# Kernel optimization log

Hardware: AMD Instinct MI355X
Metric: run time of the kernel (lower is better)

The kernel has to match this reference:

```python
import jax, jax.numpy as jnp
import numpy as np

N, C, H, W = 64, 64, 8, 8   # batch, channels (img_net_out_dim), feature-map HxW
E = 256                      # ques_rnn_hidden_dim
G = 512                      # rn_g_dim
FD = 512                     # rn_f_dim
GIN = 2 * (C + 2) + E        # g-MLP input dim = 388
NUM_CLASSES = 2


def _lin(key, din, dout):
    # kaiming-uniform-like init for a Linear stored as (in, out)
    bound = float(np.sqrt(6.0 / din))
    w = jax.random.uniform(key, (din, dout), minval=-bound, maxval=bound, dtype=jnp.float32)
    b = jnp.zeros((dout,), dtype=jnp.float32)
    return w, b


def setup_inputs() -> dict:
    key = jax.random.key(0)
    ks = jax.random.split(key, 9)
    img = jax.random.normal(ks[0], (N, C, H, W), dtype=jnp.float32)
    ques = jax.random.normal(ks[1], (N, E), dtype=jnp.float32)
    g_w1, g_b1 = _lin(ks[2], GIN, G)
    g_w2, g_b2 = _lin(ks[3], G, G)
    g_w3, g_b3 = _lin(ks[4], G, G)
    g_w4, g_b4 = _lin(ks[5], G, G)
    f_w1, f_b1 = _lin(ks[6], G, FD)
    f_w2, f_b2 = _lin(ks[7], FD, FD)
    f_w3, f_b3 = _lin(ks[8], FD, NUM_CLASSES)
    return dict(img=img, ques=ques,
                g_w1=g_w1, g_b1=g_b1, g_w2=g_w2, g_b2=g_b2,
                g_w3=g_w3, g_b3=g_b3, g_w4=g_w4, g_b4=g_b4,
                f_w1=f_w1, f_b1=f_b1, f_w2=f_w2, f_b2=f_b2,
                f_w3=f_w3, f_b3=f_b3)


def _img_to_pairs(img, ques):
    # img: (n, c, h, w), ques: (n, e) -> pairs: (n, hw*hw, 2*(c+2)+e)
    n, c, h, w = img.shape
    hw = h * w
    cells = img.reshape(n, c, hw)
    idx = jnp.arange(hw)
    loc = jnp.stack([idx // w, idx % w], axis=0).astype(img.dtype)  # (2, hw)
    cells = jnp.concatenate([cells, jnp.broadcast_to(loc[None], (n, 2, hw))], axis=1)
    feats = cells.transpose(0, 2, 1)  # (n, hw, c+2)
    fdim = feats.shape[-1]
    one = jnp.broadcast_to(feats[:, :, None, :], (n, hw, hw, fdim))   # object i
    two = jnp.broadcast_to(feats[:, None, :, :], (n, hw, hw, fdim))   # object j
    q = jnp.broadcast_to(ques[:, None, None, :], (n, hw, hw, ques.shape[-1]))
    return jnp.concatenate([one, two, q], axis=-1).reshape(n, hw * hw, -1)


def reference(img, ques, g_w1, g_b1, g_w2, g_b2, g_w3, g_b3, g_w4, g_b4,
              f_w1, f_b1, f_w2, f_b2, f_w3, f_b3):
    pairs = _img_to_pairs(img, ques)                      # (N, HW^2, GIN)
    hdd = jax.nn.relu(pairs @ g_w1 + g_b1)                # shared g-MLP over all pairs
    hdd = jax.nn.relu(hdd @ g_w2 + g_b2)
    hdd = jax.nn.relu(hdd @ g_w3 + g_b3)
    hdd = jax.nn.relu(hdd @ g_w4 + g_b4)
    context = hdd.mean(axis=1)                            # (N, G)
    z = jax.nn.relu(context @ f_w1 + f_b1)                # f-MLP (dropout = identity in eval)
    z = jax.nn.relu(z @ f_w2 + f_b2)
    scores = z @ f_w3 + f_b3                              # (N, 2)
    return jax.nn.log_softmax(scores, axis=1)
```

## Files before the change

### kernel.cpp

```cpp
#include <hip/hip_runtime.h>

typedef unsigned short u16;
typedef unsigned int u32;
typedef _Float16 f16;

using half8 = __attribute__((ext_vector_type(8))) _Float16;
using f32x4 = __attribute__((ext_vector_type(4))) float;
using f32x16 = __attribute__((ext_vector_type(16))) float;

__global__ __launch_bounds__(512) void prep_p12(const float* __restrict__ img,
                                                const float* __restrict__ gw1,
                                                float* __restrict__ P1,
                                                f16* __restrict__ P2h) {
    const int blk = blockIdx.x;
    const int n = blk >> 3;
    const int c0 = (blk & 7) * 8;
    const int t = threadIdx.x;
    __shared__ float feats[8][68];
    for (int idx = t; idx < 8 * 66; idx += 512) {
        int rr = idx / 66, cc = idx % 66, cell = c0 + rr;
        float v;
        if (cc < 64)       v = img[((size_t)(n * 64 + cc)) * 64 + cell];
        else if (cc == 64) v = (float)(cell >> 3);
        else               v = (float)(cell & 7);
        feats[rr][cc] = v;
    }
    __syncthreads();
    const int g = t;
    float a1[8], a2[8];
#pragma unroll
    for (int r = 0; r < 8; ++r) { a1[r] = 0.f; a2[r] = 0.f; }
    for (int c = 0; c < 66; ++c) {
        float wa = gw1[(size_t)c * 512 + g];
        float wb = gw1[(size_t)(66 + c) * 512 + g];
#pragma unroll
        for (int r = 0; r < 8; ++r) {
            a1[r] += feats[r][c] * wa;
            a2[r] += feats[r][c] * wb;
        }
    }
#pragma unroll
    for (int r = 0; r < 8; ++r) {
        P1[((size_t)(n * 64 + c0 + r)) * 512 + g] = a1[r];
        P2h[((size_t)(n * 64 + c0 + r)) * 512 + g] = (f16)a2[r];
    }
}

__global__ __launch_bounds__(512) void prep_q2(const float* __restrict__ ques,
                                               const float* __restrict__ gw1,
                                               const float* __restrict__ gb1,
                                               const float* __restrict__ P1,
                                               f16* __restrict__ P1h,
                                               float* __restrict__ Ctx) {
    const int n = blockIdx.x;
    const int t = threadIdx.x;
    __shared__ float q[256];
    if (t < 256) q[t] = ques[(size_t)n * 256 + t];
    __syncthreads();
    float acc = gb1[t];
    for (int e = 0; e < 256; ++e)
        acc += q[e] * gw1[(size_t)(132 + e) * 512 + t];
    const float* src = P1 + (((size_t)(n * 64)) << 9) + t;
    f16* dst = P1h + (((size_t)(n * 64)) << 9) + t;
    for (int r = 0; r < 64; ++r)
        dst[(size_t)r * 512] = (f16)(src[(size_t)r * 512] + acc);
    Ctx[(size_t)n * 512 + t] = 0.f;
}

__global__ void transpose_w(const float* __restrict__ W2, const float* __restrict__ W3,
                            const float* __restrict__ W4, f16* __restrict__ T2,
                            f16* __restrict__ T3, f16* __restrict__ T4) {
    const int L = blockIdx.z;
    const float* W = (L == 0) ? W2 : ((L == 1) ? W3 : W4);
    f16* T = (L == 0) ? T2 : ((L == 1) ? T3 : T4);
    __shared__ float tile[32][33];
    const int bx = blockIdx.x * 32;
    const int by = blockIdx.y * 32;
    const int tx = threadIdx.x, ty = threadIdx.y;
    for (int r = ty; r < 32; r += 8)
        tile[r][tx] = W[(size_t)(by + r) * 512 + bx + tx];
    __syncthreads();
    for (int r = ty; r < 32; r += 8) {
        const int n = bx + r, k = by + tx;
        T[(size_t)(k >> 4) * 8192 + ((k >> 3) & 1) * 4096 + n * 8 + (k & 7)] =
            (f16)tile[tx][r];
    }
}

__global__ __launch_bounds__(512, 4) void fused_g234(
    const f16* __restrict__ P1h, const f16* __restrict__ P2h,
    const f16* __restrict__ T2, const f16* __restrict__ T3,
    const f16* __restrict__ T4, const float* __restrict__ gb2,
    const float* __restrict__ gb3, const float* __restrict__ gb4,
    float* __restrict__ Ctx) {
    const int tid = threadIdx.x;
    const int lane = tid & 63;
    const int lane31 = lane & 31;
    const int khalf = lane >> 5;
    const int wv = tid >> 6;
    const int b = blockIdx.x;
    const int nb = b >> 6;
    const int i0 = b & 63;

    __shared__ alignas(16) f16 H[64 * 512];

    const f16* P1b = P1h + (((size_t)(nb * 64 + i0)) << 9);
    const f16* P2b = P2h + (((size_t)(nb * 64)) << 9);

    {
        const int k0 = lane * 8;
        half8 x = *(const half8*)(P1b + k0);
#pragma unroll
        for (int u = 0; u < 8; ++u) {
            int r = u * 8 + wv;
            half8 y = *(const half8*)(P2b + (((size_t)r) << 9) + k0);
            half8 s = x + y;
            s = __builtin_elementwise_max(s, (half8)(f16)0.f);
            *(half8*)&H[r * 512 + (k0 ^ ((wv & 7) << 3))] = s;
        }
    }
    __syncthreads();

    f32x16 acc[2][2];
#pragma unroll
    for (int mi = 0; mi < 2; ++mi)
#pragma unroll
        for (int ni = 0; ni < 2; ++ni)
#pragma unroll
            for (int r = 0; r < 16; ++r)
                acc[mi][ni][r] = 0.f;

    const int swz = (lane31 & 7) << 3;
    const int rbase0 = lane31 * 512;
    const int rbase1 = (32 + lane31) * 512;

    auto ldsA = [&](half8 (&a)[2], int ks) {
        const int koff = ((ks << 4) | (khalf << 3)) ^ swz;
        a[0] = *(const half8*)&H[rbase0 + koff];
        a[1] = *(const half8*)&H[rbase1 + koff];
    };
    auto ldB = [&](half8 (&bf)[2], const f16* __restrict__ T, int ks) {
        const f16* p = T + ks * 8192 + khalf * 4096 + (wv * 64 + lane31) * 8;
#pragma unroll
        for (int ni = 0; ni < 2; ++ni)
            bf[ni] = *(const half8*)(p + ni * 256);
    };
    auto mfma4 = [&](half8 (&a)[2], half8 (&bf)[2]) {
        __builtin_amdgcn_s_setprio(1);
#pragma unroll
        for (int mi = 0; mi < 2; ++mi)
#pragma unroll
            for (int ni = 0; ni < 2; ++ni)
                acc[mi][ni] = __builtin_amdgcn_mfma_f32_32x32x16_f16(
                    a[mi], bf[ni], acc[mi][ni], 0, 0, 0);
        __builtin_amdgcn_s_setprio(0);
    };

    auto run_layer = [&](const f16* __restrict__ T) {
        half8 bA[2], bB[2];
        ldB(bA, T, 0);
        for (int k2 = 0; k2 < 16; ++k2) {
            const int ks = k2 * 2;
            ldB(bB, T, ks + 1);
            {
                half8 a[2];
                ldsA(a, ks);
                mfma4(a, bA);
            }
            if (k2 < 15) ldB(bA, T, ks + 2);
            {
                half8 a[2];
                ldsA(a, ks + 1);
                mfma4(a, bB);
            }
        }
    };

    auto writeback = [&](const float* __restrict__ bias) {
        float bb[2];
#pragma unroll
        for (int ni = 0; ni < 2; ++ni)
            bb[ni] = bias[wv * 64 + ni * 32 + lane31];
        __syncthreads();
#pragma unroll
        for (int mi = 0; mi < 2; ++mi) {
#pragma unroll
            for (int ni = 0; ni < 2; ++ni) {
                const int col = wv * 64 + ni * 32 + lane31;
#pragma unroll
                for (int r = 0; r < 16; ++r) {
                    const int row = mi * 32 + (r & 3) + 4 * khalf + 8 * (r >> 2);
                    float v = fmaxf(acc[mi][ni][r] + bb[ni], 0.f);
                    H[row * 512 + (col ^ ((row & 7) << 3))] = (f16)v;
                    acc[mi][ni][r] = 0.f;
                }
            }
        }
        __syncthreads();
    };

    run_layer(T2);
    writeback(gb2);
    run_layer(T3);
    writeback(gb3);
    run_layer(T4);

#pragma unroll
    for (int ni = 0; ni < 2; ++ni) {
        const int col = wv * 64 + ni * 32 + lane31;
        float bb = gb4[col];
        float s = 0.f;
#pragma unroll
        for (int mi = 0; mi < 2; ++mi)
#pragma unroll
            for (int r = 0; r < 16; ++r)
                s += fmaxf(acc[mi][ni][r] + bb, 0.f);
        s += __shfl_xor(s, 32, 64);
        if (khalf == 0)
            atomicAdd(&Ctx[(((size_t)nb) << 9) + col], s);
    }
}

__global__ __launch_bounds__(512) void fmlp_layer(
    const float* __restrict__ In, const float* __restrict__ Wt,
    const float* __restrict__ bias, float* __restrict__ Out, float scale) {
    const int n = blockIdx.x, cs = blockIdx.y;
    const int t = threadIdx.x;
    const int col = cs * 64 + (t & 63);
    const int seg = t >> 6;
    __shared__ float a[512];
    __shared__ float red[512];
    a[t] = In[(size_t)n * 512 + t] * scale;
    __syncthreads();
    float p = 0.f;
#pragma unroll 8
    for (int i = seg * 64; i < seg * 64 + 64; ++i)
        p += a[i] * Wt[(size_t)i * 512 + col];
    red[t] = p;
    __syncthreads();
    if (t < 64) {
        float v = bias[col];
#pragma unroll
        for (int sg = 0; sg < 8; ++sg) v += red[sg * 64 + t];
        Out[(size_t)n * 512 + cs * 64 + t] = fmaxf(v, 0.f);
    }
}

__global__ __launch_bounds__(64) void fmlp_out(
    const float* __restrict__ A2, const float* __restrict__ fw3,
    const float* __restrict__ fb3, float* __restrict__ out) {
    const int n = blockIdx.x;
    const int lane = threadIdx.x;
    float s0 = 0.f, s1 = 0.f;
    for (int i = lane; i < 512; i += 64) {
        float v = A2[(size_t)n * 512 + i];
        s0 += v * fw3[i * 2];
        s1 += v * fw3[i * 2 + 1];
    }
#pragma unroll
    for (int d = 1; d < 64; d <<= 1) {
        s0 += __shfl_xor(s0, d, 64);
        s1 += __shfl_xor(s1, d, 64);
    }
    if (lane == 0) {
        s0 += fb3[0];
        s1 += fb3[1];
        float m = fmaxf(s0, s1);
        float l = logf(expf(s0 - m) + expf(s1 - m)) + m;
        out[n * 2 + 0] = s0 - l;
        out[n * 2 + 1] = s1 - l;
    }
}

extern "C" void kernel_launch(void* const* d_in, const int* in_sizes, int n_in,
                              void* d_out, int out_size, void* d_ws, size_t ws_size,
                              hipStream_t stream) {
    const float* img  = (const float*)d_in[0];
    const float* ques = (const float*)d_in[1];
    const float* gw1  = (const float*)d_in[2];
    const float* gb1  = (const float*)d_in[3];
    const float* gw2  = (const float*)d_in[4];
    const float* gb2  = (const float*)d_in[5];
    const float* gw3  = (const float*)d_in[6];
    const float* gb3  = (const float*)d_in[7];
    const float* gw4  = (const float*)d_in[8];
    const float* gb4  = (const float*)d_in[9];
    const float* fw1  = (const float*)d_in[10];
    const float* fb1  = (const float*)d_in[11];
    const float* fw2  = (const float*)d_in[12];
    const float* fb2  = (const float*)d_in[13];
    const float* fw3  = (const float*)d_in[14];
    const float* fb3  = (const float*)d_in[15];

    char* ws = (char*)d_ws;
    size_t off = 0;
    float* P1  = (float*)(ws + off); off += (size_t)4096 * 512 * 4;
    f16* P1h = (f16*)(ws + off); off += (size_t)4096 * 512 * 2;
    f16* P2h = (f16*)(ws + off); off += (size_t)4096 * 512 * 2;
    float* Ctx = (float*)(ws + off); off += (size_t)64 * 512 * 4;
    float* Z1  = (float*)(ws + off); off += (size_t)64 * 512 * 4;
    float* Z2  = (float*)(ws + off); off += (size_t)64 * 512 * 4;
    f16* T2 = (f16*)(ws + off); off += (size_t)512 * 512 * 2;
    f16* T3 = (f16*)(ws + off); off += (size_t)512 * 512 * 2;
    f16* T4 = (f16*)(ws + off); off += (size_t)512 * 512 * 2;

    prep_p12<<<512, 512, 0, stream>>>(img, gw1, P1, P2h);
    prep_q2<<<64, 512, 0, stream>>>(ques, gw1, gb1, P1, P1h, Ctx);
    transpose_w<<<dim3(16, 16, 3), dim3(32, 8), 0, stream>>>(gw2, gw3, gw4, T2, T3, T4);

    fused_g234<<<4096, 512, 0, stream>>>(P1h, P2h, T2, T3, T4, gb2, gb3, gb4, Ctx);

    fmlp_layer<<<dim3(64, 8), 512, 0, stream>>>(Ctx, fw1, fb1, Z1, 1.0f / 4096.0f);
    fmlp_layer<<<dim3(64, 8), 512, 0, stream>>>(Z1, fw2, fb2, Z2, 1.0f);
    fmlp_out<<<64, 64, 0, stream>>>(Z2, fw3, fb3, (float*)d_out);
}
```

Before: 563.6 us.

## Store pair activations in MFMA k-chunked layout for contiguous LDS fragment reads

The P1/P2 half-precision buffers and the shared activation tile H move from row-major to a k-chunked (ks, khalf, row, 8) layout with an XOR swizzle on the row index. MFMA A-fragment loads become contiguous 16-byte reads, which is meant to cut LDS bank conflicts, and the writeback and prep kernels are changed to match. The two-stage B prefetch loop is also replaced with a simpler single-step prefetch loop unrolled by 2. H is now declared as 64*1024 halves although only half of that is indexed. This doubles LDS per block and may halve resident blocks per CU.

```diff
diff --git a/kernel.cpp b/kernel.cpp
--- a/kernel.cpp
+++ b/kernel.cpp
@@ -8,10 +8,11 @@
 using f32x4 = __attribute__((ext_vector_type(4))) float;
 using f32x16 = __attribute__((ext_vector_type(16))) float;
 
+
 __global__ __launch_bounds__(512) void prep_p12(const float* __restrict__ img,
                                                 const float* __restrict__ gw1,
                                                 float* __restrict__ P1,
-                                                f16* __restrict__ P2h) {
+                                                f16* __restrict__ P2c) {
     const int blk = blockIdx.x;
     const int n = blk >> 3;
     const int c0 = (blk & 7) * 8;
@@ -39,10 +40,11 @@
             a2[r] += feats[r][c] * wb;
         }
     }
+    const size_t cb = (size_t)n * 32768 + (g >> 4) * 1024 + ((g >> 3) & 1) * 512 + (g & 7);
 #pragma unroll
     for (int r = 0; r < 8; ++r) {
         P1[((size_t)(n * 64 + c0 + r)) * 512 + g] = a1[r];
-        P2h[((size_t)(n * 64 + c0 + r)) * 512 + g] = (f16)a2[r];
+        P2c[cb + (c0 + r) * 8] = (f16)a2[r];
     }
 }
 
@@ -50,7 +52,7 @@
                                                const float* __restrict__ gw1,
                                                const float* __restrict__ gb1,
                                                const float* __restrict__ P1,
-                                               f16* __restrict__ P1h,
+                                               f16* __restrict__ P1c,
                                                float* __restrict__ Ctx) {
     const int n = blockIdx.x;
     const int t = threadIdx.x;
@@ -61,9 +63,9 @@
     for (int e = 0; e < 256; ++e)
         acc += q[e] * gw1[(size_t)(132 + e) * 512 + t];
     const float* src = P1 + (((size_t)(n * 64)) << 9) + t;
-    f16* dst = P1h + (((size_t)(n * 64)) << 9) + t;
+    const size_t cb = (size_t)n * 32768 + (t >> 4) * 1024 + ((t >> 3) & 1) * 512 + (t & 7);
     for (int r = 0; r < 64; ++r)
-        dst[(size_t)r * 512] = (f16)(src[(size_t)r * 512] + acc);
+        P1c[cb + r * 8] = (f16)(src[(size_t)r * 512] + acc);
     Ctx[(size_t)n * 512 + t] = 0.f;
 }
 
@@ -88,7 +90,7 @@
 }
 
 __global__ __launch_bounds__(512, 4) void fused_g234(
-    const f16* __restrict__ P1h, const f16* __restrict__ P2h,
+    const f16* __restrict__ P1c, const f16* __restrict__ P2c,
     const f16* __restrict__ T2, const f16* __restrict__ T3,
     const f16* __restrict__ T4, const float* __restrict__ gb2,
     const float* __restrict__ gb3, const float* __restrict__ gb4,
@@ -102,21 +104,23 @@
     const int nb = b >> 6;
     const int i0 = b & 63;
 
-    __shared__ alignas(16) f16 H[64 * 512];
-
-    const f16* P1b = P1h + (((size_t)(nb * 64 + i0)) << 9);
-    const f16* P2b = P2h + (((size_t)(nb * 64)) << 9);
-
-    {
-        const int k0 = lane * 8;
-        half8 x = *(const half8*)(P1b + k0);
-#pragma unroll
-        for (int u = 0; u < 8; ++u) {
-            int r = u * 8 + wv;
-            half8 y = *(const half8*)(P2b + (((size_t)r) << 9) + k0);
+    __shared__ alignas(16) f16 H[64 * 1024];
+
+    const f16* P1b = P1c + (size_t)nb * 32768;
+    const f16* P2b = P2c + (size_t)nb * 32768;
+
+#pragma unroll
+    for (int u = 0; u < 4; ++u) {
+        const int ks = wv * 4 + u;
+        const int cb = ks * 1024 + khalf * 512;
+        const int f = ((ks & 1) << 1) | khalf;
+        half8 x = *(const half8*)(P1b + cb + i0 * 8);
+#pragma unroll
+        for (int rr = 0; rr < 2; ++rr) {
+            half8 y = *(const half8*)(P2b + cb + (rr * 32 + lane31) * 8);
             half8 s = x + y;
             s = __builtin_elementwise_max(s, (half8)(f16)0.f);
-            *(half8*)&H[r * 512 + (k0 ^ ((wv & 7) << 3))] = s;
+            *(half8*)&H[cb + (rr * 32 + (lane31 ^ f)) * 8] = s;
         }
     }
     __syncthreads();
@@ -130,14 +134,11 @@
             for (int r = 0; r < 16; ++r)
                 acc[mi][ni][r] = 0.f;
 
-    const int swz = (lane31 & 7) << 3;
-    const int rbase0 = lane31 * 512;
-    const int rbase1 = (32 + lane31) * 512;
-
     auto ldsA = [&](half8 (&a)[2], int ks) {
-        const int koff = ((ks << 4) | (khalf << 3)) ^ swz;
-        a[0] = *(const half8*)&H[rbase0 + koff];
-        a[1] = *(const half8*)&H[rbase1 + koff];
+        const int f = ((ks & 1) << 1) | khalf;
+        const int base = ks * 1024 + khalf * 512 + (lane31 ^ f) * 8;
+        a[0] = *(const half8*)&H[base];
+        a[1] = *(const half8*)&H[base + 256];
     };
     auto ldB = [&](half8 (&bf)[2], const f16* __restrict__ T, int ks) {
         const f16* p = T + ks * 8192 + khalf * 4096 + (wv * 64 + lane31) * 8;
@@ -157,22 +158,15 @@
     };
 
     auto run_layer = [&](const f16* __restrict__ T) {
-        half8 bA[2], bB[2];
-        ldB(bA, T, 0);
-        for (int k2 = 0; k2 < 16; ++k2) {
-            const int ks = k2 * 2;
-            ldB(bB, T, ks + 1);
-            {
-                half8 a[2];
-                ldsA(a, ks);
-                mfma4(a, bA);
-            }
-            if (k2 < 15) ldB(bA, T, ks + 2);
-            {
-                half8 a[2];
-                ldsA(a, ks + 1);
-                mfma4(a, bB);
-            }
+        half8 bfn[2];
+        ldB(bfn, T, 0);
+#pragma unroll 2
+        for (int ks = 0; ks < 32; ++ks) {
+            half8 bf[2] = {bfn[0], bfn[1]};
+            if (ks < 31) ldB(bfn, T, ks + 1);
+            half8 a[2];
+            ldsA(a, ks);
+            mfma4(a, bf);
         }
     };
 
@@ -183,15 +177,18 @@
             bb[ni] = bias[wv * 64 + ni * 32 + lane31];
         __syncthreads();
 #pragma unroll
-        for (int mi = 0; mi < 2; ++mi) {
-#pragma unroll
-            for (int ni = 0; ni < 2; ++ni) {
-                const int col = wv * 64 + ni * 32 + lane31;
+        for (int ni = 0; ni < 2; ++ni) {
+            const int c = wv * 64 + ni * 32 + lane31;
+            const int cbase = (c >> 4) * 1024 + ((c >> 3) & 1) * 512;
+            const int fw = (((c >> 4) & 1) << 1) | ((c >> 3) & 1);
+            const int j = c & 7;
+#pragma unroll
+            for (int mi = 0; mi < 2; ++mi) {
 #pragma unroll
                 for (int r = 0; r < 16; ++r) {
                     const int row = mi * 32 + (r & 3) + 4 * khalf + 8 * (r >> 2);
                     float v = fmaxf(acc[mi][ni][r] + bb[ni], 0.f);
-                    H[row * 512 + (col ^ ((row & 7) << 3))] = (f16)v;
+                    H[cbase + (row ^ fw) * 8 + j] = (f16)v;
                     acc[mi][ni][r] = 0.f;
                 }
             }
@@ -295,8 +292,8 @@
     char* ws = (char*)d_ws;
     size_t off = 0;
     float* P1  = (float*)(ws + off); off += (size_t)4096 * 512 * 4;
-    f16* P1h = (f16*)(ws + off); off += (size_t)4096 * 512 * 2;
-    f16* P2h = (f16*)(ws + off); off += (size_t)4096 * 512 * 2;
+    f16* P1c = (f16*)(ws + off); off += (size_t)4096 * 512 * 2;
+    f16* P2c = (f16*)(ws + off); off += (size_t)4096 * 512 * 2;
     float* Ctx = (float*)(ws + off); off += (size_t)64 * 512 * 4;
     float* Z1  = (float*)(ws + off); off += (size_t)64 * 512 * 4;
     float* Z2  = (float*)(ws + off); off += (size_t)64 * 512 * 4;
@@ -304,11 +301,11 @@
     f16* T3 = (f16*)(ws + off); off += (size_t)512 * 512 * 2;
     f16* T4 = (f16*)(ws + off); off += (size_t)512 * 512 * 2;
 
-    prep_p12<<<512, 512, 0, stream>>>(img, gw1, P1, P2h);
-    prep_q2<<<64, 512, 0, stream>>>(ques, gw1, gb1, P1, P1h, Ctx);
+    prep_p12<<<512, 512, 0, stream>>>(img, gw1, P1, P2c);
+    prep_q2<<<64, 512, 0, stream>>>(ques, gw1, gb1, P1, P1c, Ctx);
     transpose_w<<<dim3(16, 16, 3), dim3(32, 8), 0, stream>>>(gw2, gw3, gw4, T2, T3, T4);
 
-    fused_g234<<<4096, 512, 0, stream>>>(P1h, P2h, T2, T3, T4, gb2, gb3, gb4, Ctx);
+    fused_g234<<<4096, 512, 0, stream>>>(P1c, P2c, T2, T3, T4, gb2, gb3, gb4, Ctx);
 
     fmlp_layer<<<dim3(64, 8), 512, 0, stream>>>(Ctx, fw1, fb1, Z1, 1.0f / 4096.0f);
     fmlp_layer<<<dim3(64, 8), 512, 0, stream>>>(Z1, fw2, fb2, Z2, 1.0f);
```

New measurement: 559.3 us. About the same (-0.8%).
